# Performance work log

Hardware: AMD Instinct MI355X
Metric: run time of the kernel (lower is better)

The kernel has to match this reference:

```python
import jax, jax.numpy as jnp
import numpy as np

B, S, D = 2, 2048, 2048
H, KVH, HD = 16, 4, 128
E, TOPK, FF = 8, 2, 4096
EPS = 1e-6
THETA = 1000000.0


def setup_inputs() -> dict:
    key = jax.random.key(0)
    ks = jax.random.split(key, 12)
    s = 0.02
    return {
        'hidden_states': jax.random.normal(ks[0], (B, S, D), jnp.float32),
        'attention_mask': jnp.ones((B, S), dtype=bool),
        'wq': jax.random.normal(ks[1], (D, H * HD), jnp.float32) * s,
        'wk': jax.random.normal(ks[2], (D, KVH * HD), jnp.float32) * s,
        'wv': jax.random.normal(ks[3], (D, KVH * HD), jnp.float32) * s,
        'wo': jax.random.normal(ks[4], (H * HD, D), jnp.float32) * s,
        'ln1_w': jnp.ones((D,), jnp.float32),
        'ln2_w': jnp.ones((D,), jnp.float32),
        'gate_w': jax.random.normal(ks[5], (D, E), jnp.float32) * s,
        'w_gate': jax.random.normal(ks[6], (E, D, FF), jnp.float32) * s,
        'w_up': jax.random.normal(ks[7], (E, D, FF), jnp.float32) * s,
        'w_down': jax.random.normal(ks[8], (E, FF, D), jnp.float32) * s,
    }


def rms_norm(x, w):
    xf = x.astype(jnp.float32)
    var = jnp.mean(jnp.square(xf), axis=-1, keepdims=True)
    return w * (xf * jax.lax.rsqrt(var + EPS)).astype(x.dtype)


def rotate_half(x):
    x1, x2 = x[..., : x.shape[-1] // 2], x[..., x.shape[-1] // 2 :]
    return jnp.concatenate((-x2, x1), axis=-1)


def attention(x, mask, wq, wk, wv, wo):
    q = (x @ wq).reshape(B, S, H, HD)
    k = (x @ wk).reshape(B, S, KVH, HD)
    v = (x @ wv).reshape(B, S, KVH, HD)
    # RoPE (fp32 freqs, as in MixtralRotaryEmbedding)
    inv_freq = 1.0 / (THETA ** (jnp.arange(0, HD, 2, dtype=jnp.float32) / HD))
    freqs = jnp.arange(S, dtype=jnp.float32)[:, None] * inv_freq[None, :]  # [S, HD/2]
    emb = jnp.concatenate([freqs, freqs], axis=-1)  # [S, HD]
    cos = jnp.cos(emb)[None, :, None, :]  # [1,S,1,HD]
    sin = jnp.sin(emb)[None, :, None, :]
    q = q * cos + rotate_half(q) * sin
    k = k * cos + rotate_half(k) * sin
    # GQA: repeat kv heads
    k = jnp.repeat(k, H // KVH, axis=2)
    v = jnp.repeat(v, H // KVH, axis=2)
    # faithful to source: keep-mask is triu(ones, k=1) (strictly-above-diagonal)
    causal = jnp.triu(jnp.ones((S, S), dtype=bool), k=1)
    combined = mask[:, None, None, :] & causal[None, None, :, :]  # [B,1,S,S]
    neg = jnp.finfo(jnp.float32).min
    bias = jnp.where(combined, 0.0, neg).astype(jnp.float32)
    scores = jnp.einsum('bqhd,bkhd->bhqk', q, k) * (HD ** -0.5) + bias
    attn = jax.nn.softmax(scores, axis=-1)
    out = jnp.einsum('bhqk,bkhd->bqhd', attn, v).reshape(B, S, H * HD)
    return out @ wo


def moe(x, gate_w, w_gate, w_up, w_down):
    # x: [T, D]
    T = x.shape[0]
    logits = x.astype(jnp.float32) @ gate_w  # fp32 router, [T, E]
    rw = jax.nn.softmax(logits, axis=-1)
    top_w, top_i = jax.lax.top_k(rw, TOPK)
    top_w = top_w / jnp.sum(top_w, axis=-1, keepdims=True)
    w_full = jnp.zeros((T, E), jnp.float32).at[jnp.arange(T)[:, None], top_i].set(top_w)
    out = jnp.zeros_like(x)
    for e in range(E):  # small fixed expert loop
        h = jax.nn.silu(x @ w_gate[e]) * (x @ w_up[e])
        out = out + w_full[:, e, None] * (h @ w_down[e])
    return out


def reference(hidden_states, attention_mask, wq, wk, wv, wo, ln1_w, ln2_w, gate_w, w_gate, w_up, w_down):
    residual = hidden_states
    h = rms_norm(hidden_states, ln1_w)
    h = residual + attention(h, attention_mask, wq, wk, wv, wo)
    residual = h
    h = rms_norm(h, ln2_w)
    m = moe(h.reshape(-1, D), gate_w, w_gate, w_up, w_down).reshape(B, S, D)
    return residual + m
```

## Files before the change

kernel.cpp:

```cpp
#include <hip/hip_runtime.h>
#include <cstdint>
#include <cstddef>


typedef unsigned short u16;
typedef __attribute__((ext_vector_type(8))) short short8;
typedef __attribute__((ext_vector_type(8))) _Float16 half8;
typedef __attribute__((ext_vector_type(8))) __bf16 bf16x8;
typedef __attribute__((ext_vector_type(4))) float f32x4;
typedef __attribute__((ext_vector_type(4))) u16 us4;
typedef __attribute__((ext_vector_type(4))) unsigned int u32x4;

__device__ __forceinline__ u16 f2bf(float f) {
  unsigned u = __builtin_bit_cast(unsigned, f);
  u += 0x7fffu + ((u >> 16) & 1u);
  return (u16)(u >> 16);
}
__device__ __forceinline__ void splitf16(float x, float scale, u16 &hi, u16 &lo) {
  float xs = x * scale;
  _Float16 h = (_Float16)xs;
  hi = __builtin_bit_cast(u16, h);
  _Float16 l = (_Float16)(xs - (float)h);
  lo = __builtin_bit_cast(u16, l);
}
__device__ __forceinline__ f32x4 mma_bf(short8 a, short8 b, f32x4 c) {
  return __builtin_amdgcn_mfma_f32_16x16x32_bf16(
      __builtin_bit_cast(bf16x8, a), __builtin_bit_cast(bf16x8, b), c, 0, 0, 0);
}
__device__ __forceinline__ f32x4 mma_h(short8 a, short8 b, f32x4 c) {
  return __builtin_amdgcn_mfma_f32_16x16x32_f16(
      __builtin_bit_cast(half8, a), __builtin_bit_cast(half8, b), c, 0, 0, 0);
}
__device__ __forceinline__ void gl16(const u16 *g, u16 *l) {
  __builtin_amdgcn_global_load_lds(
      (const __attribute__((address_space(1))) unsigned *)g,
      (__attribute__((address_space(3))) unsigned *)l, 16, 0, 0);
}

template <int OM>
__global__ __launch_bounds__(256) void k_trans(
    const float *__restrict__ src, u16 *__restrict__ d0, u16 *__restrict__ d1,
    int ld_src, int ld_dst, long long zhi, long long zlo, int zmod,
    long long dstz, int inter, float scale) {
  int z = blockIdx.z;
  src += (long long)(z / zmod) * zhi + (long long)(z % zmod) * zlo;
  d0 += (long long)z * dstz;
  if constexpr (OM == 1) d1 += (long long)z * dstz;
  int r0 = blockIdx.y * 64, c0 = blockIdx.x * 64;
  __shared__ float t[64][65];
  int tx = threadIdx.x;
  int rr = tx >> 4, cc = (tx & 15) * 4;
#pragma unroll
  for (int i = 0; i < 4; i++) {
    float4 v = *(const float4 *)(src + (size_t)(r0 + rr + i * 16) * ld_src + c0 + cc);
    t[rr + i * 16][cc] = v.x; t[rr + i * 16][cc + 1] = v.y;
    t[rr + i * 16][cc + 2] = v.z; t[rr + i * 16][cc + 3] = v.w;
  }
  __syncthreads();
#pragma unroll
  for (int i = 0; i < 4; i++) {
    int c = rr + i * 16;
    int f = c0 + c;
    int drow = (inter < 0) ? f : (((f >> 5) << 6) + (f & 31) + (inter << 5));
    size_t bo = (size_t)drow * ld_dst + r0 + cc;
    if constexpr (OM == 0) {
      us4 o;
#pragma unroll
      for (int j = 0; j < 4; j++) o[j] = f2bf(t[cc + j][c]);
      *(us4 *)(d0 + bo) = o;
    } else {
      us4 oh, ol;
#pragma unroll
      for (int j = 0; j < 4; j++) {
        u16 a, b; splitf16(t[cc + j][c], scale, a, b);
        oh[j] = a; ol[j] = b;
      }
      *(us4 *)(d0 + bo) = oh;
      *(us4 *)(d1 + bo) = ol;
    }
  }
}

__global__ __launch_bounds__(256) void k_rms(
    const float *__restrict__ x, const float *__restrict__ w,
    u16 *__restrict__ oh, u16 *__restrict__ ol, float scale16) {
  int row = blockIdx.x, tid = threadIdx.x;
  const float *xr = x + (size_t)row * 2048;
  float4 v0 = *(const float4 *)(xr + tid * 8);
  float4 v1 = *(const float4 *)(xr + tid * 8 + 4);
  float ss = v0.x * v0.x + v0.y * v0.y + v0.z * v0.z + v0.w * v0.w +
             v1.x * v1.x + v1.y * v1.y + v1.z * v1.z + v1.w * v1.w;
  __shared__ float red[256];
  red[tid] = ss;
  __syncthreads();
  for (int s = 128; s > 0; s >>= 1) {
    if (tid < s) red[tid] += red[tid + s];
    __syncthreads();
  }
  float sc = rsqrtf(red[0] * (1.0f / 2048.0f) + 1e-6f);
  float4 w0 = *(const float4 *)(w + tid * 8);
  float4 w1 = *(const float4 *)(w + tid * 8 + 4);
  float o[8] = {v0.x * sc * w0.x, v0.y * sc * w0.y, v0.z * sc * w0.z, v0.w * sc * w0.w,
                v1.x * sc * w1.x, v1.y * sc * w1.y, v1.z * sc * w1.z, v1.w * sc * w1.w};
  size_t bo = (size_t)row * 2048 + tid * 8;
  if (ol) {
    us4 h0, h1, l0, l1;
#pragma unroll
    for (int j = 0; j < 4; j++) {
      u16 a, b;
      splitf16(o[j], scale16, a, b); h0[j] = a; l0[j] = b;
      splitf16(o[j + 4], scale16, a, b); h1[j] = a; l1[j] = b;
    }
    *(us4 *)(oh + bo) = h0; *(us4 *)(oh + bo + 4) = h1;
    *(us4 *)(ol + bo) = l0; *(us4 *)(ol + bo + 4) = l1;
  } else {
    us4 a, b;
#pragma unroll
    for (int j = 0; j < 4; j++) { a[j] = f2bf(o[j]); b[j] = f2bf(o[j + 4]); }
    *(us4 *)(oh + bo) = a; *(us4 *)(oh + bo + 4) = b;
  }
}

__global__ void k_cs(float2 *__restrict__ cs) {
  int idx = blockIdx.x * 256 + threadIdx.x;
  int s = idx >> 6, i = idx & 63;
  double inv = exp2(-(double)i * (19.931568569324174 / 64.0));
  double ang = (double)s * inv;
  cs[idx] = make_float2((float)cos(ang), (float)sin(ang));
}

__global__ __launch_bounds__(256) void k_rope(
    const float *__restrict__ qkv, const float2 *__restrict__ cs,
    u16 *__restrict__ qh, u16 *__restrict__ ql,
    u16 *__restrict__ kh, u16 *__restrict__ kl) {
  int t = blockIdx.x, tid = threadIdx.x;
  int s = t & 2047;
  const float *bp = qkv + (size_t)t * 3072;
  for (int p = tid; p < 1024; p += 256) {
    int hh = p >> 6, i = p & 63;
    float2 c = cs[s * 64 + i];
    float x1 = bp[hh * 128 + i], x2 = bp[hh * 128 + 64 + i];
    float o1 = x1 * c.x - x2 * c.y, o2 = x2 * c.x + x1 * c.y;
    size_t b1 = (size_t)t * 2048 + hh * 128 + i;
    u16 a, b;
    splitf16(o1, 16.f, a, b); qh[b1] = a; ql[b1] = b;
    splitf16(o2, 16.f, a, b); qh[b1 + 64] = a; ql[b1 + 64] = b;
  }
  {
    int hh = tid >> 6, i = tid & 63;
    float2 c = cs[s * 64 + i];
    float x1 = bp[2048 + hh * 128 + i], x2 = bp[2048 + hh * 128 + 64 + i];
    float o1 = x1 * c.x - x2 * c.y, o2 = x2 * c.x + x1 * c.y;
    size_t b1 = (size_t)t * 512 + hh * 128 + i;
    u16 a, b;
    splitf16(o1, 16.f, a, b); kh[b1] = a; kl[b1] = b;
    splitf16(o2, 16.f, a, b); kh[b1 + 64] = a; kl[b1 + 64] = b;
  }
}

__global__ __launch_bounds__(512, 4) void k_attn(
    const u16 *__restrict__ qh, const u16 *__restrict__ ql,
    const u16 *__restrict__ kh, const u16 *__restrict__ kl,
    const u16 *__restrict__ vh, const u16 *__restrict__ vl,
    u16 *__restrict__ oh, u16 *__restrict__ ol) {
  const int qx = blockIdx.x, kvh = blockIdx.y, b = blockIdx.z;
  const int qt = (b == 0) ? qx : 63 - qx;
  const int q0 = qt * 32;
  const int tid = threadIdx.x, wid = tid >> 6, lane = tid & 63;
  const int hq = wid & 3, rh = wid >> 2;
  const int h = kvh * 4 + hq;
  const int lr = lane & 15, g = lane >> 4, lk = g * 8;
  const float SC = 0.08838834764831845f * 1.44269504088896341f / 256.0f;

  __shared__ alignas(16) u16 KT[2][2][4096];
  __shared__ alignas(16) u16 VT[2][2][4096];
  __shared__ alignas(16) u16 Pb[8][2][512];

  short8 qfh[4], qfl[4];
  {
    size_t qo = (size_t)(b * 2048 + q0 + rh * 16 + lr) * 2048 + h * 128 + lk;
#pragma unroll
    for (int c = 0; c < 4; c++) {
      qfh[c] = *(const short8 *)(qh + qo + c * 32);
      qfl[c] = *(const short8 *)(ql + qo + c * 32);
    }
  }
  f32x4 accO[8] = {};
  float m_r[4], l_r[4];
#pragma unroll
  for (int r = 0; r < 4; r++) { m_r[r] = -3.0e38f; l_r[r] = 0.f; }

  const int kv_start = q0;
  const int nIter = (2048 - kv_start) >> 5;

  const u16 *khp = kh + (size_t)(b * 2048) * 512 + kvh * 128;
  const u16 *klp = kl + (size_t)(b * 2048) * 512 + kvh * 128;
  const u16 *vhp = vh + ((size_t)(b * 4 + kvh) * 128) * 2048;
  const u16 *vlp = vl + ((size_t)(b * 4 + kvh) * 128) * 2048;

  auto stage = [&](int bf, int kv0) {
    const int c0 = wid * 64;
    const int cc = tid;
    const int krow = cc >> 4, kcol = (cc & 15) ^ (krow & 7);
    const size_t kg = (size_t)(kv0 + krow) * 512 + kcol * 8;
    gl16(khp + kg, &KT[bf][0][c0 * 8]);
    gl16(klp + kg, &KT[bf][1][c0 * 8]);
    const int vd = cc >> 2, vi = (cc & 3) ^ (vd & 3);
    const size_t vg = (size_t)vd * 2048 + kv0 + vi * 8;
    gl16(vhp + vg, &VT[bf][0][c0 * 8]);
    gl16(vlp + vg, &VT[bf][1][c0 * 8]);
  };

  stage(0, kv_start);
  __syncthreads();
  int buf = 0;
  for (int it = 0; it < nIter; it++) {
    const int kv0 = kv_start + (it << 5);
    if (it + 1 < nIter) stage(buf ^ 1, kv0 + 32);
    f32x4 s0 = {}, s1 = {};
    {
      const u16 *KhL = KT[buf][0], *KlL = KT[buf][1];
#pragma unroll
      for (int c = 0; c < 4; c++) {
        const int idx0 = lr * 128 + (((c * 4 + g) ^ (lr & 7)) << 3);
        const int idx1 = idx0 + 2048;
        short8 k0h = *(const short8 *)(KhL + idx0);
        short8 k0l = *(const short8 *)(KlL + idx0);
        short8 k1h = *(const short8 *)(KhL + idx1);
        short8 k1l = *(const short8 *)(KlL + idx1);
        s0 = mma_h(qfh[c], k0h, s0); s0 = mma_h(qfh[c], k0l, s0); s0 = mma_h(qfl[c], k0h, s0);
        s1 = mma_h(qfh[c], k1h, s1); s1 = mma_h(qfh[c], k1l, s1); s1 = mma_h(qfl[c], k1h, s1);
      }
    }
    const bool msk = (kv0 <= q0 + 31);
    float alpha[4];
#pragma unroll
    for (int r = 0; r < 4; r++) {
      float v0 = s0[r] * SC, v1 = s1[r] * SC;
      if (msk) {
        int rowq = q0 + rh * 16 + g * 4 + r;
        if (kv0 + lr <= rowq) v0 = -3.0e38f;
        if (kv0 + 16 + lr <= rowq) v1 = -3.0e38f;
      }
      float mx = fmaxf(v0, v1);
#pragma unroll
      for (int o = 1; o < 16; o <<= 1) mx = fmaxf(mx, __shfl_xor(mx, o));
      float mn = fmaxf(m_r[r], mx);
      float p0 = exp2f(v0 - mn), p1 = exp2f(v1 - mn);
      float sum = p0 + p1;
#pragma unroll
      for (int o = 1; o < 16; o <<= 1) sum += __shfl_xor(sum, o);
      alpha[r] = exp2f(m_r[r] - mn);
      l_r[r] = l_r[r] * alpha[r] + sum;
      m_r[r] = mn;
      const int prow = g * 4 + r;
      {
        int c0l = lr, c1l = 16 + lr;
        int p0i = prow * 32 + ((c0l & 7) | ((((c0l >> 3) ^ g) & 3) << 3));
        int p1i = prow * 32 + ((c1l & 7) | ((((c1l >> 3) ^ g) & 3) << 3));
        u16 x, y;
        splitf16(p0, 16.f, x, y); Pb[wid][0][p0i] = x; Pb[wid][1][p0i] = y;
        splitf16(p1, 16.f, x, y); Pb[wid][0][p1i] = x; Pb[wid][1][p1i] = y;
      }
    }
#pragma unroll
    for (int nt = 0; nt < 8; nt++) {
      f32x4 t = accO[nt];
      t[0] *= alpha[0]; t[1] *= alpha[1]; t[2] *= alpha[2]; t[3] *= alpha[3];
      accO[nt] = t;
    }
    asm volatile("s_waitcnt lgkmcnt(0)" ::: "memory");
    const int pidx = lr * 32 + (((g ^ (lr >> 2)) & 3) << 3);
    short8 pfh = *(const short8 *)(&Pb[wid][0][pidx]);
    short8 pfl = *(const short8 *)(&Pb[wid][1][pidx]);
    {
      const u16 *VhL = VT[buf][0], *VlL = VT[buf][1];
#pragma unroll
      for (int nt = 0; nt < 8; nt++) {
        const int d = nt * 16 + lr;
        const int vidx = d * 32 + (((g ^ (d & 3)) & 3) << 3);
        short8 wfh = *(const short8 *)(VhL + vidx);
        short8 wfl = *(const short8 *)(VlL + vidx);
        f32x4 t = accO[nt];
        t = mma_h(pfh, wfh, t); t = mma_h(pfh, wfl, t); t = mma_h(pfl, wfh, t);
        accO[nt] = t;
      }
    }
    __syncthreads();
    buf ^= 1;
  }
  float inv[4];
#pragma unroll
  for (int r = 0; r < 4; r++) inv[r] = 1.0f / (l_r[r] * 256.0f);
#pragma unroll
  for (int nt = 0; nt < 8; nt++)
#pragma unroll
    for (int r = 0; r < 4; r++) {
      float v = accO[nt][r] * inv[r];
      size_t idx = (size_t)(b * 2048 + q0 + rh * 16 + g * 4 + r) * 2048 + h * 128 + nt * 16 + lr;
      u16 x, y; splitf16(v, 16.f, x, y);
      oh[idx] = x; ol[idx] = y;
    }
}

__global__ __launch_bounds__(256) void k_fixrow(
    const u16 *__restrict__ vh, const u16 *__restrict__ vl,
    u16 *__restrict__ oh, u16 *__restrict__ ol) {
  const int bg = blockIdx.x >> 4, dg = blockIdx.x & 15;
  const int tid = threadIdx.x, lane = tid & 63, w = tid >> 6;
  __shared__ float part[4][8];
#pragma unroll
  for (int i = 0; i < 8; i++) {
    size_t ro = ((size_t)(bg * 128 + dg * 8 + i)) * 2048 + tid * 8;
    short8 a = *(const short8 *)(vh + ro);
    short8 c = *(const short8 *)(vl + ro);
    float s = 0.f;
#pragma unroll
    for (int j = 0; j < 8; j++)
      s += (float)__builtin_bit_cast(_Float16, (u16)a[j]) +
           (float)__builtin_bit_cast(_Float16, (u16)c[j]);
#pragma unroll
    for (int o = 1; o < 64; o <<= 1) s += __shfl_xor(s, o);
    if (lane == 0) part[w][i] = s;
  }
  __syncthreads();
  if (tid < 8) {
    float tot = part[0][tid] + part[1][tid] + part[2][tid] + part[3][tid];
    float v = tot * (1.0f / 32768.0f);
    u16 x, y; splitf16(v, 16.f, x, y);
    int bb = bg >> 2, kvh = bg & 3;
#pragma unroll
    for (int hq2 = 0; hq2 < 4; hq2++) {
      size_t idx = ((size_t)(bb * 2048 + 2047)) * 2048 + (kvh * 4 + hq2) * 128 + dg * 8 + tid;
      oh[idx] = x; ol[idx] = y;
    }
  }
}

template <int MODE>
__global__ __launch_bounds__(256) void k_gemm(
    const u16 *__restrict__ Ah, const u16 *__restrict__ Al,
    const u16 *__restrict__ Bh, const u16 *__restrict__ Bl,
    int M, int N, int K, int lda, int ldb, int ldc, float descale,
    float *__restrict__ outf, const float *__restrict__ resid) {
  const int tid = threadIdx.x;
  const int wid = tid >> 6, lane = tid & 63;
  const int wr = wid >> 1, wc = wid & 1;
  const int l15 = lane & 15, l4 = lane >> 4;
  const int n0 = blockIdx.x * 128, m0 = blockIdx.y * 128;
  __shared__ alignas(16) u16 AsH[4096], BsH[4096];
  __shared__ alignas(16) u16 AsL[4096], BsL[4096];
  const int r16 = lane >> 2, c8 = (lane & 3) << 3;
  int a0 = m0 + wid * 16 + r16, a1 = a0 + 64;
  const u16 *pa0 = Ah + (size_t)a0 * lda + c8;
  const u16 *pa1 = Ah + (size_t)a1 * lda + c8;
  const int b0 = n0 + wid * 16 + r16, b1 = b0 + 64;
  const u16 *pb0 = Bh + (size_t)b0 * ldb + c8;
  const u16 *pb1 = Bh + (size_t)b1 * ldb + c8;
  const u16 *qa0 = Al + (size_t)a0 * lda + c8;
  const u16 *qa1 = Al + (size_t)a1 * lda + c8;
  const u16 *qb0 = Bl + (size_t)b0 * ldb + c8;
  const u16 *qb1 = Bl + (size_t)b1 * ldb + c8;
  u16 *sa0 = AsH + wid * 512, *sa1 = AsH + 2048 + wid * 512;
  u16 *sb0 = BsH + wid * 512, *sb1 = BsH + 2048 + wid * 512;
  f32x4 acc[4][4] = {};
  const int fa = (wr * 64 + l15) * 32 + (l4 << 3);
  const int fb = (wc * 64 + l15) * 32 + (l4 << 3);
  for (int k0 = 0; k0 < K; k0 += 32) {
    gl16(pa0 + k0, sa0); gl16(pa1 + k0, sa1);
    gl16(pb0 + k0, sb0); gl16(pb1 + k0, sb1);
    gl16(qa0 + k0, AsL + wid * 512); gl16(qa1 + k0, AsL + 2048 + wid * 512);
    gl16(qb0 + k0, BsL + wid * 512); gl16(qb1 + k0, BsL + 2048 + wid * 512);
    __syncthreads();
    short8 ah[4], bh[4], al[4], bl[4];
#pragma unroll
    for (int i = 0; i < 4; i++) ah[i] = *(const short8 *)(AsH + fa + i * 512);
#pragma unroll
    for (int i = 0; i < 4; i++) bh[i] = *(const short8 *)(BsH + fb + i * 512);
#pragma unroll
    for (int i = 0; i < 4; i++) al[i] = *(const short8 *)(AsL + fa + i * 512);
#pragma unroll
    for (int i = 0; i < 4; i++) bl[i] = *(const short8 *)(BsL + fb + i * 512);
#pragma unroll
    for (int mi = 0; mi < 4; mi++)
#pragma unroll
      for (int ni = 0; ni < 4; ni++) {
        f32x4 c = acc[mi][ni];
        c = mma_h(ah[mi], bh[ni], c);
        c = mma_h(ah[mi], bl[ni], c);
        c = mma_h(al[mi], bh[ni], c);
        acc[mi][ni] = c;
      }
    __syncthreads();
  }
#pragma unroll
  for (int mi = 0; mi < 4; mi++)
#pragma unroll
    for (int q = 0; q < 4; q++) {
      int row = m0 + wr * 64 + l4 * 4 + mi * 16 + q;
      size_t rb = (size_t)row * ldc;
#pragma unroll
      for (int ni = 0; ni < 4; ni++) {
        int col = n0 + wc * 64 + ni * 16 + l15;
        float v = acc[mi][ni][q] * descale;
        if constexpr (MODE == 1) v += resid[rb + col];
        outf[rb + col] = v;
      }
    }
}

template <int MODE>
__global__ __launch_bounds__(512, 1) void k_gemm8(
    const u16 *__restrict__ A, const u16 *__restrict__ Ball,
    int N, int K, int lda, int ldb, int ldc,
    float *__restrict__ outf, u16 *__restrict__ outh,
    const int *__restrict__ offs, const int *__restrict__ counts,
    const int *__restrict__ row_token, const float *__restrict__ row_w) {
  const int e = blockIdx.z;
  const int seg = offs[e], cnt = counts[e];
  const int m0 = blockIdx.y * 256;
  if (m0 >= cnt) return;
  const int n0 = blockIdx.x * 256;
  const u16 *B = Ball + (size_t)e * (size_t)N * (size_t)ldb;
  const int tid = threadIdx.x, wid = tid >> 6, lane = tid & 63;
  const int wr = wid >> 2, wc = wid & 3;
  const int l15 = lane & 15, l4 = lane >> 4;

  __shared__ alignas(16) u16 Ls[4][2][8192];

  const u16 *pA[2], *pB[2];
#pragma unroll
  for (int j = 0; j < 2; j++) {
    int s = (wid * 2 + j) * 64 + lane;
    int row = s >> 2;
    int kc = (s & 3) ^ ((row >> 1) & 3);
    int ra = m0 + row; if (ra > cnt - 1) ra = cnt - 1;
    pA[j] = A + (size_t)(seg + ra) * lda + kc * 8;
    pB[j] = B + (size_t)(n0 + row) * ldb + kc * 8;
  }
  int offA[8], offB[4];
#pragma unroll
  for (int mi = 0; mi < 8; mi++) {
    int r = wr * 128 + mi * 16 + l15;
    offA[mi] = (r * 4 + (l4 ^ ((r >> 1) & 3))) << 3;
  }
#pragma unroll
  for (int ni = 0; ni < 4; ni++) {
    int r = wc * 64 + ni * 16 + l15;
    offB[ni] = (r * 4 + (l4 ^ ((r >> 1) & 3))) << 3;
  }

  f32x4 acc[8][4] = {};
  const int nT = K >> 5;
  auto stage = [&](int t, int j) {
    gl16(pA[j] + (t << 5), &Ls[t & 3][0][(wid * 2 + j) << 9]);
    gl16(pB[j] + (t << 5), &Ls[t & 3][1][(wid * 2 + j) << 9]);
  };
  stage(0, 0); stage(0, 1); stage(1, 0); stage(1, 1);
  asm volatile("s_waitcnt vmcnt(4)" ::: "memory");
  __builtin_amdgcn_sched_barrier(0);
  __builtin_amdgcn_s_barrier();
  __builtin_amdgcn_sched_barrier(0);

  short8 bf[4], af0[4], af1[4];
  for (int t = 0; t < nT; t++) {
    const u16 *LA = &Ls[t & 3][0][0], *LB = &Ls[t & 3][1][0];
#pragma unroll
    for (int i = 0; i < 4; i++) bf[i] = *(const short8 *)(LB + offB[i]);
#pragma unroll
    for (int i = 0; i < 4; i++) af0[i] = *(const short8 *)(LA + offA[i]);
    if (t + 2 < nT) stage(t + 2, 0);
    asm volatile("s_waitcnt lgkmcnt(0)" ::: "memory");
    __builtin_amdgcn_sched_barrier(0);
    __builtin_amdgcn_s_setprio(1);
#pragma unroll
    for (int mi = 0; mi < 4; mi++)
#pragma unroll
      for (int ni = 0; ni < 4; ni++)
        acc[mi][ni] = mma_bf(af0[mi], bf[ni], acc[mi][ni]);
    __builtin_amdgcn_s_setprio(0);
#pragma unroll
    for (int i = 0; i < 4; i++) af1[i] = *(const short8 *)(LA + offA[4 + i]);
    if (t + 2 < nT) stage(t + 2, 1);
    asm volatile("s_waitcnt lgkmcnt(0)" ::: "memory");
    __builtin_amdgcn_sched_barrier(0);
    __builtin_amdgcn_s_setprio(1);
#pragma unroll
    for (int mi = 0; mi < 4; mi++)
#pragma unroll
      for (int ni = 0; ni < 4; ni++)
        acc[4 + mi][ni] = mma_bf(af1[mi], bf[ni], acc[4 + mi][ni]);
    __builtin_amdgcn_s_setprio(0);
    if (t + 1 < nT) {
      if (t + 2 < nT) {
        asm volatile("s_waitcnt vmcnt(4)" ::: "memory");
      } else {
        asm volatile("s_waitcnt vmcnt(0)" ::: "memory");
      }
      __builtin_amdgcn_sched_barrier(0);
      __builtin_amdgcn_s_barrier();
      __builtin_amdgcn_sched_barrier(0);
    }
  }

  if constexpr (MODE == 2) {
    const int f0 = (n0 + wc * 64) >> 1;
#pragma unroll
    for (int mi = 0; mi < 8; mi++)
#pragma unroll
      for (int q = 0; q < 4; q++) {
        int rl = m0 + wr * 128 + mi * 16 + l4 * 4 + q;
        if (rl < cnt) {
          size_t rb = (size_t)(seg + rl) * ldc;
#pragma unroll
          for (int nt = 0; nt < 2; nt++) {
            float g = acc[mi][nt][q], u = acc[mi][nt + 2][q];
            float hv = (g / (1.0f + __expf(-g))) * u;
            outh[rb + f0 + nt * 16 + l15] = f2bf(hv);
          }
        }
      }
  } else {
#pragma unroll
    for (int mi = 0; mi < 8; mi++)
#pragma unroll
      for (int q = 0; q < 4; q++) {
        int rl = m0 + wr * 128 + mi * 16 + l4 * 4 + q;
        if (rl < cnt) {
          int tok = row_token[seg + rl];
          float w = row_w[seg + rl];
          size_t rb = (size_t)tok * ldc;
#pragma unroll
          for (int ni = 0; ni < 4; ni++)
            atomicAdd(outf + rb + n0 + wc * 64 + ni * 16 + l15,
                      w * acc[mi][ni][q]);
        }
      }
  }
}

__global__ __launch_bounds__(64) void k_router(
    const float *__restrict__ hb, const float *__restrict__ w2,
    const float *__restrict__ gw, int *__restrict__ topi,
    float *__restrict__ topw, int *__restrict__ counts) {
  const int t = blockIdx.x, lane = threadIdx.x;
  const float *xr = hb + (size_t)t * 2048;
  float xs[32];
  float ss = 0.f;
#pragma unroll
  for (int c = 0; c < 8; c++) {
    float4 v = *(const float4 *)(xr + c * 256 + lane * 4);
    xs[c * 4 + 0] = v.x; xs[c * 4 + 1] = v.y; xs[c * 4 + 2] = v.z; xs[c * 4 + 3] = v.w;
    ss += v.x * v.x + v.y * v.y + v.z * v.z + v.w * v.w;
  }
#pragma unroll
  for (int o = 1; o < 64; o <<= 1) ss += __shfl_xor(ss, o);
  const float sc = rsqrtf(ss * (1.0f / 2048.0f) + 1e-6f);
  float acc[8] = {0, 0, 0, 0, 0, 0, 0, 0};
#pragma unroll
  for (int c = 0; c < 8; c++)
#pragma unroll
    for (int j = 0; j < 4; j++) {
      int d = c * 256 + lane * 4 + j;
      float xn = xs[c * 4 + j] * sc * w2[d];
      float4 g0 = *(const float4 *)(gw + (size_t)d * 8);
      float4 g1 = *(const float4 *)(gw + (size_t)d * 8 + 4);
      acc[0] += xn * g0.x; acc[1] += xn * g0.y; acc[2] += xn * g0.z; acc[3] += xn * g0.w;
      acc[4] += xn * g1.x; acc[5] += xn * g1.y; acc[6] += xn * g1.z; acc[7] += xn * g1.w;
    }
#pragma unroll
  for (int e = 0; e < 8; e++) {
    float v = acc[e];
#pragma unroll
    for (int o = 1; o < 64; o <<= 1) v += __shfl_xor(v, o);
    acc[e] = v;
  }
  if (lane == 0) {
    float mx = acc[0];
#pragma unroll
    for (int e = 1; e < 8; e++) mx = fmaxf(mx, acc[e]);
    float p[8];
#pragma unroll
    for (int e = 0; e < 8; e++) p[e] = __expf(acc[e] - mx);
    int e0 = 0;
#pragma unroll
    for (int e = 1; e < 8; e++) if (p[e] > p[e0]) e0 = e;
    int e1 = (e0 == 0) ? 1 : 0;
#pragma unroll
    for (int e = 0; e < 8; e++) if (e != e0 && p[e] > p[e1]) e1 = e;
    float s2 = p[e0] + p[e1];
    topi[t * 2] = e0; topi[t * 2 + 1] = e1;
    topw[t * 2] = p[e0] / s2; topw[t * 2 + 1] = p[e1] / s2;
    atomicAdd(counts + e0, 1);
    atomicAdd(counts + e1, 1);
  }
}

__global__ void k_zero(int *__restrict__ p) {
  if (threadIdx.x < 8) p[threadIdx.x] = 0;
}
__global__ void k_offsets(const int *__restrict__ counts, int *__restrict__ offs,
                          int *__restrict__ cursors) {
  if (threadIdx.x == 0) {
    int o = 0;
    for (int e = 0; e < 8; e++) { offs[e] = o; o += counts[e]; cursors[e] = 0; }
    offs[8] = o;
  }
}
__global__ __launch_bounds__(256) void k_scatter(
    const int *__restrict__ topi, const float *__restrict__ topw,
    const int *__restrict__ offs, int *__restrict__ cursors,
    int *__restrict__ row_token, float *__restrict__ row_w) {
  int t = blockIdx.x * 256 + threadIdx.x;
  if (t >= 4096) return;
#pragma unroll
  for (int s = 0; s < 2; s++) {
    int e = topi[t * 2 + s];
    int pos = offs[e] + atomicAdd(cursors + e, 1);
    row_token[pos] = t;
    row_w[pos] = topw[t * 2 + s];
  }
}
__global__ __launch_bounds__(256) void k_gather(
    const u16 *__restrict__ h2, const int *__restrict__ row_token,
    u16 *__restrict__ xg) {
  int r = blockIdx.x;
  int t = row_token[r];
  ((u32x4 *)(xg + (size_t)r * 2048))[threadIdx.x] =
      ((const u32x4 *)(h2 + (size_t)t * 2048))[threadIdx.x];
}

extern "C" void kernel_launch(void *const *d_in, const int *in_sizes, int n_in,
                              void *d_out, int out_size, void *d_ws,
                              size_t ws_size, hipStream_t stream) {
  const float *hidden = (const float *)d_in[0];
  const float *wq = (const float *)d_in[2];
  const float *wk = (const float *)d_in[3];
  const float *wv = (const float *)d_in[4];
  const float *wo = (const float *)d_in[5];
  const float *ln1 = (const float *)d_in[6];
  const float *ln2 = (const float *)d_in[7];
  const float *gw = (const float *)d_in[8];
  const float *wg = (const float *)d_in[9];
  const float *wu = (const float *)d_in[10];
  const float *wd = (const float *)d_in[11];
  float *out = (float *)d_out;

  char *base = (char *)d_ws;
  size_t off = 0;
  auto alloc = [&](size_t bytes) -> char * {
    char *p = base + off;
    off += (bytes + 255) & ~(size_t)255;
    return p;
  };
  u16 *wqkvTh = (u16 *)alloc((size_t)3072 * 2048 * 2);
  u16 *wqkvTl = (u16 *)alloc((size_t)3072 * 2048 * 2);
  u16 *woTh = (u16 *)alloc((size_t)2048 * 2048 * 2);
  u16 *woTl = (u16 *)alloc((size_t)2048 * 2048 * 2);
  u16 *wguT = (u16 *)alloc((size_t)8 * 8192 * 2048 * 2);
  u16 *wdT = (u16 *)alloc((size_t)8 * 2048 * 4096 * 2);
  u16 *h1h = (u16 *)alloc((size_t)4096 * 2048 * 2);
  u16 *h1l = (u16 *)alloc((size_t)4096 * 2048 * 2);
  float *qkv = (float *)alloc((size_t)4096 * 3072 * 4);
  u16 *qbh = (u16 *)alloc((size_t)4096 * 2048 * 2);
  u16 *qbl = (u16 *)alloc((size_t)4096 * 2048 * 2);
  u16 *kbh = (u16 *)alloc((size_t)4096 * 512 * 2);
  u16 *kbl = (u16 *)alloc((size_t)4096 * 512 * 2);
  u16 *vth = (u16 *)alloc((size_t)8 * 128 * 2048 * 2);
  u16 *vtl = (u16 *)alloc((size_t)8 * 128 * 2048 * 2);
  float2 *cs = (float2 *)alloc((size_t)2048 * 64 * 8);
  u16 *aoh = (u16 *)alloc((size_t)4096 * 2048 * 2);
  u16 *aol = (u16 *)alloc((size_t)4096 * 2048 * 2);
  u16 *h2 = (u16 *)alloc((size_t)4096 * 2048 * 2);
  int *topi = (int *)alloc(4096 * 2 * 4);
  float *topwt = (float *)alloc(4096 * 2 * 4);
  int *counts = (int *)alloc(64 * 4);
  int *offs = (int *)alloc(64 * 4);
  int *cursors = (int *)alloc(64 * 4);
  int *row_token = (int *)alloc(8192 * 4);
  float *row_w = (float *)alloc(8192 * 4);
  u16 *xg = (u16 *)alloc((size_t)8192 * 2048 * 2);
  u16 *Hb = (u16 *)alloc((size_t)8192 * 4096 * 2);
  if (off > ws_size) return;

  dim3 T256(256), T64(64);
  k_cs<<<dim3(512), T256, 0, stream>>>(cs);
  k_trans<1><<<dim3(32, 32, 1), T256, 0, stream>>>(wq, wqkvTh, wqkvTl, 2048, 2048, 0, 0, 1, 0, -1, 256.f);
  k_trans<1><<<dim3(8, 32, 1), T256, 0, stream>>>(wk, wqkvTh + (size_t)2048 * 2048, wqkvTl + (size_t)2048 * 2048, 512, 2048, 0, 0, 1, 0, -1, 256.f);
  k_trans<1><<<dim3(8, 32, 1), T256, 0, stream>>>(wv, wqkvTh + (size_t)2560 * 2048, wqkvTl + (size_t)2560 * 2048, 512, 2048, 0, 0, 1, 0, -1, 256.f);
  k_trans<1><<<dim3(32, 32, 1), T256, 0, stream>>>(wo, woTh, woTl, 2048, 2048, 0, 0, 1, 0, -1, 256.f);
  k_trans<0><<<dim3(64, 32, 8), T256, 0, stream>>>(wg, wguT, nullptr, 4096, 2048, (long long)2048 * 4096, 0, 1, (long long)8192 * 2048, 0, 1.f);
  k_trans<0><<<dim3(64, 32, 8), T256, 0, stream>>>(wu, wguT, nullptr, 4096, 2048, (long long)2048 * 4096, 0, 1, (long long)8192 * 2048, 1, 1.f);
  k_trans<0><<<dim3(32, 64, 8), T256, 0, stream>>>(wd, wdT, nullptr, 2048, 4096, (long long)4096 * 2048, 0, 1, (long long)2048 * 4096, -1, 1.f);
  k_rms<<<dim3(4096), T256, 0, stream>>>(hidden, ln1, h1h, h1l, 16.f);
  k_gemm<0><<<dim3(24, 32, 1), T256, 0, stream>>>(
      h1h, h1l, wqkvTh, wqkvTl, 4096, 3072, 2048, 2048, 2048, 3072,
      1.f / 4096.f, qkv, nullptr);
  k_rope<<<dim3(4096), T256, 0, stream>>>(qkv, cs, qbh, qbl, kbh, kbl);
  k_trans<1><<<dim3(2, 32, 8), T256, 0, stream>>>(qkv + 2560, vth, vtl, 3072, 2048, (long long)2048 * 3072, 128, 4, (long long)128 * 2048, -1, 16.f);
  k_attn<<<dim3(64, 4, 2), dim3(512), 0, stream>>>(qbh, qbl, kbh, kbl, vth, vtl, aoh, aol);
  k_fixrow<<<dim3(128), T256, 0, stream>>>(vth, vtl, aoh, aol);
  k_gemm<1><<<dim3(16, 32, 1), T256, 0, stream>>>(
      aoh, aol, woTh, woTl, 4096, 2048, 2048, 2048, 2048, 2048,
      1.f / 4096.f, out, hidden);
  k_rms<<<dim3(4096), T256, 0, stream>>>(out, ln2, h2, nullptr, 1.f);
  k_zero<<<dim3(1), T64, 0, stream>>>(counts);
  k_router<<<dim3(4096), T64, 0, stream>>>(out, ln2, gw, topi, topwt, counts);
  k_offsets<<<dim3(1), dim3(1), 0, stream>>>(counts, offs, cursors);
  k_scatter<<<dim3(16), T256, 0, stream>>>(topi, topwt, offs, cursors, row_token, row_w);
  k_gather<<<dim3(8192), T256, 0, stream>>>(h2, row_token, xg);
  k_gemm8<2><<<dim3(32, 16, 8), dim3(512), 0, stream>>>(
      xg, wguT, 8192, 2048, 2048, 2048, 4096,
      nullptr, Hb, offs, counts, nullptr, nullptr);
  k_gemm8<3><<<dim3(8, 16, 8), dim3(512), 0, stream>>>(
      Hb, wdT, 2048, 4096, 4096, 4096, 2048,
      out, nullptr, offs, counts, row_token, row_w);
  (void)in_sizes; (void)n_in; (void)out_size;
}
```

Baseline: 1.523 ms.

## Rewrite split-fp16 dense GEMM with 4-stage LDS pipeline and 8 waves

Replaces the single-buffered 256-thread split-half GEMM used for the QKV and output projections with a 512-thread kernel. It keeps a 4-deep ring of LDS tiles, issues global-to-LDS loads two tiles ahead, and uses explicit vmcnt/lgkmcnt waits plus one barrier per K step instead of two. LDS rows are XOR-swizzled to avoid bank conflicts, and MFMA sections are raised in priority with s_setprio. The kernel is meant to hide global load latency behind the three-MFMA error-compensated product. In exchange it uses 128 KB of LDS and one block per CU, and it depends on hand-tuned wait counts being correct.

```diff
diff --git a/kernel.cpp b/kernel.cpp
--- a/kernel.cpp
+++ b/kernel.cpp
@@ -338,70 +338,118 @@
 }
 
 template <int MODE>
-__global__ __launch_bounds__(256) void k_gemm(
+__global__ __launch_bounds__(512, 1) void k_gemmS(
     const u16 *__restrict__ Ah, const u16 *__restrict__ Al,
     const u16 *__restrict__ Bh, const u16 *__restrict__ Bl,
-    int M, int N, int K, int lda, int ldb, int ldc, float descale,
+    int K, int lda, int ldb, int ldc, float descale,
     float *__restrict__ outf, const float *__restrict__ resid) {
-  const int tid = threadIdx.x;
-  const int wid = tid >> 6, lane = tid & 63;
-  const int wr = wid >> 1, wc = wid & 1;
+  const int n0 = blockIdx.x * 128, m0 = blockIdx.y * 128;
+  const int tid = threadIdx.x, wid = tid >> 6, lane = tid & 63;
+  const int wr = wid >> 2, wc = wid & 3;
   const int l15 = lane & 15, l4 = lane >> 4;
-  const int n0 = blockIdx.x * 128, m0 = blockIdx.y * 128;
-  __shared__ alignas(16) u16 AsH[4096], BsH[4096];
-  __shared__ alignas(16) u16 AsL[4096], BsL[4096];
-  const int r16 = lane >> 2, c8 = (lane & 3) << 3;
-  int a0 = m0 + wid * 16 + r16, a1 = a0 + 64;
-  const u16 *pa0 = Ah + (size_t)a0 * lda + c8;
-  const u16 *pa1 = Ah + (size_t)a1 * lda + c8;
-  const int b0 = n0 + wid * 16 + r16, b1 = b0 + 64;
-  const u16 *pb0 = Bh + (size_t)b0 * ldb + c8;
-  const u16 *pb1 = Bh + (size_t)b1 * ldb + c8;
-  const u16 *qa0 = Al + (size_t)a0 * lda + c8;
-  const u16 *qa1 = Al + (size_t)a1 * lda + c8;
-  const u16 *qb0 = Bl + (size_t)b0 * ldb + c8;
-  const u16 *qb1 = Bl + (size_t)b1 * ldb + c8;
-  u16 *sa0 = AsH + wid * 512, *sa1 = AsH + 2048 + wid * 512;
-  u16 *sb0 = BsH + wid * 512, *sb1 = BsH + 2048 + wid * 512;
-  f32x4 acc[4][4] = {};
-  const int fa = (wr * 64 + l15) * 32 + (l4 << 3);
-  const int fb = (wc * 64 + l15) * 32 + (l4 << 3);
-  for (int k0 = 0; k0 < K; k0 += 32) {
-    gl16(pa0 + k0, sa0); gl16(pa1 + k0, sa1);
-    gl16(pb0 + k0, sb0); gl16(pb1 + k0, sb1);
-    gl16(qa0 + k0, AsL + wid * 512); gl16(qa1 + k0, AsL + 2048 + wid * 512);
-    gl16(qb0 + k0, BsL + wid * 512); gl16(qb1 + k0, BsL + 2048 + wid * 512);
-    __syncthreads();
-    short8 ah[4], bh[4], al[4], bl[4];
-#pragma unroll
-    for (int i = 0; i < 4; i++) ah[i] = *(const short8 *)(AsH + fa + i * 512);
-#pragma unroll
-    for (int i = 0; i < 4; i++) bh[i] = *(const short8 *)(BsH + fb + i * 512);
-#pragma unroll
-    for (int i = 0; i < 4; i++) al[i] = *(const short8 *)(AsL + fa + i * 512);
-#pragma unroll
-    for (int i = 0; i < 4; i++) bl[i] = *(const short8 *)(BsL + fb + i * 512);
-#pragma unroll
-    for (int mi = 0; mi < 4; mi++)
-#pragma unroll
-      for (int ni = 0; ni < 4; ni++) {
+
+  __shared__ alignas(16) u16 Ls[4][4][4096];
+
+  const int s = wid * 64 + lane;
+  const int row = s >> 2;
+  const int kc = (s & 3) ^ ((row >> 1) & 3);
+  const u16 *pS[4];
+  pS[0] = Ah + (size_t)(m0 + row) * lda + kc * 8;
+  pS[1] = Al + (size_t)(m0 + row) * lda + kc * 8;
+  pS[2] = Bh + (size_t)(n0 + row) * ldb + kc * 8;
+  pS[3] = Bl + (size_t)(n0 + row) * ldb + kc * 8;
+
+  int offA[4], offB[2];
+#pragma unroll
+  for (int mi = 0; mi < 4; mi++) {
+    int r = wr * 64 + mi * 16 + l15;
+    offA[mi] = (r * 4 + (l4 ^ ((r >> 1) & 3))) << 3;
+  }
+#pragma unroll
+  for (int ni = 0; ni < 2; ni++) {
+    int r = wc * 32 + ni * 16 + l15;
+    offB[ni] = (r * 4 + (l4 ^ ((r >> 1) & 3))) << 3;
+  }
+
+  f32x4 acc[4][2] = {};
+  const int nT = K >> 5;
+  auto stage = [&](int t, int x) {
+    gl16(pS[x] + (t << 5), &Ls[t & 3][x][wid << 9]);
+  };
+  stage(0, 0); stage(0, 1); stage(0, 2); stage(0, 3);
+  stage(1, 0); stage(1, 1); stage(1, 2); stage(1, 3);
+  asm volatile("s_waitcnt vmcnt(4)" ::: "memory");
+  __builtin_amdgcn_sched_barrier(0);
+  __builtin_amdgcn_s_barrier();
+  __builtin_amdgcn_sched_barrier(0);
+
+  short8 bh[2], bl[2], ah[2], al[2], ah2[2], al2[2];
+  for (int t = 0; t < nT; t++) {
+    const u16 *LAh = &Ls[t & 3][0][0], *LAl = &Ls[t & 3][1][0];
+    const u16 *LBh = &Ls[t & 3][2][0], *LBl = &Ls[t & 3][3][0];
+#pragma unroll
+    for (int i = 0; i < 2; i++) {
+      bh[i] = *(const short8 *)(LBh + offB[i]);
+      bl[i] = *(const short8 *)(LBl + offB[i]);
+      ah[i] = *(const short8 *)(LAh + offA[i]);
+      al[i] = *(const short8 *)(LAl + offA[i]);
+    }
+    if (t + 2 < nT) { stage(t + 2, 0); stage(t + 2, 1); }
+    asm volatile("s_waitcnt lgkmcnt(0)" ::: "memory");
+    __builtin_amdgcn_sched_barrier(0);
+    __builtin_amdgcn_s_setprio(1);
+#pragma unroll
+    for (int mi = 0; mi < 2; mi++)
+#pragma unroll
+      for (int ni = 0; ni < 2; ni++) {
         f32x4 c = acc[mi][ni];
         c = mma_h(ah[mi], bh[ni], c);
         c = mma_h(ah[mi], bl[ni], c);
         c = mma_h(al[mi], bh[ni], c);
         acc[mi][ni] = c;
       }
-    __syncthreads();
-  }
+    __builtin_amdgcn_s_setprio(0);
+#pragma unroll
+    for (int i = 0; i < 2; i++) {
+      ah2[i] = *(const short8 *)(LAh + offA[2 + i]);
+      al2[i] = *(const short8 *)(LAl + offA[2 + i]);
+    }
+    if (t + 2 < nT) { stage(t + 2, 2); stage(t + 2, 3); }
+    asm volatile("s_waitcnt lgkmcnt(0)" ::: "memory");
+    __builtin_amdgcn_sched_barrier(0);
+    __builtin_amdgcn_s_setprio(1);
+#pragma unroll
+    for (int mi = 0; mi < 2; mi++)
+#pragma unroll
+      for (int ni = 0; ni < 2; ni++) {
+        f32x4 c = acc[2 + mi][ni];
+        c = mma_h(ah2[mi], bh[ni], c);
+        c = mma_h(ah2[mi], bl[ni], c);
+        c = mma_h(al2[mi], bh[ni], c);
+        acc[2 + mi][ni] = c;
+      }
+    __builtin_amdgcn_s_setprio(0);
+    if (t + 1 < nT) {
+      if (t + 2 < nT) {
+        asm volatile("s_waitcnt vmcnt(4)" ::: "memory");
+      } else {
+        asm volatile("s_waitcnt vmcnt(0)" ::: "memory");
+      }
+      __builtin_amdgcn_sched_barrier(0);
+      __builtin_amdgcn_s_barrier();
+      __builtin_amdgcn_sched_barrier(0);
+    }
+  }
+
 #pragma unroll
   for (int mi = 0; mi < 4; mi++)
 #pragma unroll
     for (int q = 0; q < 4; q++) {
-      int row = m0 + wr * 64 + l4 * 4 + mi * 16 + q;
-      size_t rb = (size_t)row * ldc;
-#pragma unroll
-      for (int ni = 0; ni < 4; ni++) {
-        int col = n0 + wc * 64 + ni * 16 + l15;
+      int rowo = m0 + wr * 64 + mi * 16 + l4 * 4 + q;
+      size_t rb = (size_t)rowo * ldc;
+#pragma unroll
+      for (int ni = 0; ni < 2; ni++) {
+        int col = n0 + wc * 32 + ni * 16 + l15;
         float v = acc[mi][ni][q] * descale;
         if constexpr (MODE == 1) v += resid[rb + col];
         outf[rb + col] = v;
@@ -693,15 +741,15 @@
   k_trans<0><<<dim3(64, 32, 8), T256, 0, stream>>>(wu, wguT, nullptr, 4096, 2048, (long long)2048 * 4096, 0, 1, (long long)8192 * 2048, 1, 1.f);
   k_trans<0><<<dim3(32, 64, 8), T256, 0, stream>>>(wd, wdT, nullptr, 2048, 4096, (long long)4096 * 2048, 0, 1, (long long)2048 * 4096, -1, 1.f);
   k_rms<<<dim3(4096), T256, 0, stream>>>(hidden, ln1, h1h, h1l, 16.f);
-  k_gemm<0><<<dim3(24, 32, 1), T256, 0, stream>>>(
-      h1h, h1l, wqkvTh, wqkvTl, 4096, 3072, 2048, 2048, 2048, 3072,
+  k_gemmS<0><<<dim3(24, 32), dim3(512), 0, stream>>>(
+      h1h, h1l, wqkvTh, wqkvTl, 2048, 2048, 2048, 3072,
       1.f / 4096.f, qkv, nullptr);
   k_rope<<<dim3(4096), T256, 0, stream>>>(qkv, cs, qbh, qbl, kbh, kbl);
   k_trans<1><<<dim3(2, 32, 8), T256, 0, stream>>>(qkv + 2560, vth, vtl, 3072, 2048, (long long)2048 * 3072, 128, 4, (long long)128 * 2048, -1, 16.f);
   k_attn<<<dim3(64, 4, 2), dim3(512), 0, stream>>>(qbh, qbl, kbh, kbl, vth, vtl, aoh, aol);
   k_fixrow<<<dim3(128), T256, 0, stream>>>(vth, vtl, aoh, aol);
-  k_gemm<1><<<dim3(16, 32, 1), T256, 0, stream>>>(
-      aoh, aol, woTh, woTl, 4096, 2048, 2048, 2048, 2048, 2048,
+  k_gemmS<1><<<dim3(16, 32), dim3(512), 0, stream>>>(
+      aoh, aol, woTh, woTl, 2048, 2048, 2048, 2048,
       1.f / 4096.f, out, hidden);
   k_rms<<<dim3(4096), T256, 0, stream>>>(out, ln2, h2, nullptr, 1.f);
   k_zero<<<dim3(1), T64, 0, stream>>>(counts);
```

Result: no change. 1.535 ms (+0.8%).
